# Kernel tuning notes

Hardware: AMD Instinct MI355X
Metric: run time of the kernel (lower is better)

The kernel has to match this reference:

```python
import jax, jax.numpy as jnp
import numpy as np

N_NODES = 40000
N_EDGES = 640000
F_IN = 128
HID = 128
N_CLASSES = 10
N_GRAPHS = 64


def _gcn_conv(x, row, col, norm, W, b, n_nodes):
    h = x @ W                                   # [N, H]
    msg = h[row] * norm[:, None]                # [E+N, H] gather + scale
    out = jax.ops.segment_sum(msg, col, num_segments=n_nodes)  # scatter-add
    return out + b


def setup_inputs() -> dict:
    key = jax.random.key(0)
    ks = jax.random.split(key, 8)
    x = jax.random.normal(ks[0], (N_NODES, F_IN), dtype=jnp.float32)
    edge_index = jax.random.randint(ks[1], (2, N_EDGES), 0, N_NODES, dtype=jnp.int32)
    batch = jnp.sort(jax.random.randint(ks[2], (N_NODES,), 0, N_GRAPHS, dtype=jnp.int32))
    s1 = 1.0 / np.sqrt(F_IN)
    s2 = 1.0 / np.sqrt(HID)
    W1 = jax.random.normal(ks[3], (F_IN, HID), dtype=jnp.float32) * s1
    W2 = jax.random.normal(ks[4], (HID, HID), dtype=jnp.float32) * s2
    W3 = jax.random.normal(ks[5], (HID, HID), dtype=jnp.float32) * s2
    Wl = jax.random.normal(ks[6], (HID, N_CLASSES), dtype=jnp.float32) * s2
    b1 = jnp.zeros((HID,), jnp.float32)
    b2 = jnp.zeros((HID,), jnp.float32)
    b3 = jnp.zeros((HID,), jnp.float32)
    bl = jnp.zeros((N_CLASSES,), jnp.float32)
    return {"x": x, "edge_index": edge_index, "batch": batch,
            "W1": W1, "b1": b1, "W2": W2, "b2": b2, "W3": W3, "b3": b3,
            "Wl": Wl, "bl": bl}


def reference(x, edge_index, batch, W1, b1, W2, b2, W3, b3, Wl, bl):
    n = x.shape[0]
    # add self-loops (PyG add_remaining_self_loops with weight 1)
    loops = jnp.arange(n, dtype=edge_index.dtype)
    row = jnp.concatenate([edge_index[0], loops])
    col = jnp.concatenate([edge_index[1], loops])
    w = jnp.ones(row.shape, dtype=x.dtype)
    # symmetric normalization: deg over target nodes incl. self-loops
    deg = jax.ops.segment_sum(w, col, num_segments=n)
    dis = jnp.where(deg > 0, jax.lax.rsqrt(deg), 0.0)
    norm = dis[row] * dis[col]                  # [E+N]

    h = jax.nn.relu(_gcn_conv(x, row, col, norm, W1, b1, n))
    h = jax.nn.relu(_gcn_conv(h, row, col, norm, W2, b2, n))
    h = jax.nn.relu(_gcn_conv(h, row, col, norm, W3, b3, n))

    # global mean pool over graph ids
    sums = jax.ops.segment_sum(h, batch, num_segments=N_GRAPHS)      # [G, H]
    cnts = jax.ops.segment_sum(jnp.ones((n,), h.dtype), batch, num_segments=N_GRAPHS)
    pooled = sums / jnp.maximum(cnts, 1.0)[:, None]
    # dropout(p=0.2) is identity in eval mode
    return pooled @ Wl + bl                     # [G, num_classes]
```

## Files before the change

kernel.cpp:

```cpp
#include <hip/hip_runtime.h>
#include <hip/hip_bf16.h>

#define N_NODES   40000
#define N_EDGES   640000
#define F         128
#define N_GRAPHS  64
#define N_CLASSES 10

typedef short bf16x8 __attribute__((ext_vector_type(8)));
typedef float f32x4  __attribute__((ext_vector_type(4)));

__device__ __forceinline__ unsigned short f2bf(float f) {
    union { float f; unsigned u; } v; v.f = f;
    unsigned r = v.u + 0x7fffu + ((v.u >> 16) & 1u);
    return (unsigned short)(r >> 16);
}
__device__ __forceinline__ float bflo(unsigned u) { return __uint_as_float(u << 16); }
__device__ __forceinline__ float bfhi(unsigned u) { return __uint_as_float(u & 0xffff0000u); }
__device__ __forceinline__ unsigned pack2(float a, float b) {
    return (unsigned)f2bf(a) | ((unsigned)f2bf(b) << 16);
}

#define APITCH 136

__global__ void wcvt_kernel(const float* __restrict__ W1, const float* __restrict__ W2,
                            const float* __restrict__ W3, unsigned short* __restrict__ Wt,
                            int* __restrict__ deg) {
    int idx = blockIdx.x * 256 + threadIdx.x;
    if (idx < N_NODES) deg[idx] = 0;
    int l = idx >> 14;
    int r = idx & 16383;
    int c = r >> 7, k = r & 127;
    const float* W = (l == 0) ? W1 : ((l == 1) ? W2 : W3);
    Wt[idx] = f2bf(W[k * 128 + c]);
}

__global__ __launch_bounds__(1024) void scan_kernel(
    const int* __restrict__ deg, int* __restrict__ rowptr,
    int* __restrict__ cursor, float* __restrict__ dis,
    float* __restrict__ pooled_zero) {
    __shared__ int wsum[16];
    __shared__ int tile_total_s;
    const int tid  = threadIdx.x;
    const int lane = tid & 63;
    const int wave = tid >> 6;

    for (int k = tid; k < N_GRAPHS * F + N_GRAPHS; k += 1024) pooled_zero[k] = 0.f;

    int running = 0;
    for (int t = 0; t < 10; ++t) {
        const int base = t * 4096 + tid * 4;
        int4 d = make_int4(0, 0, 0, 0);
        if (base < N_NODES) d = *(const int4*)(deg + base);
        const int sown = d.x + d.y + d.z + d.w;

        int s = sown;
#pragma unroll
        for (int off = 1; off < 64; off <<= 1) {
            int n = __shfl_up(s, off, 64);
            if (lane >= off) s += n;
        }
        if (lane == 63) wsum[wave] = s;
        __syncthreads();

        if (wave == 0) {
            int v = (lane < 16) ? wsum[lane] : 0;
#pragma unroll
            for (int off = 1; off < 16; off <<= 1) {
                int n = __shfl_up(v, off, 64);
                if (lane >= off) v += n;
            }
            if (lane < 16) wsum[lane] = v;
            if (lane == 15) tile_total_s = v;
        }
        __syncthreads();

        int excl = running + (wave ? wsum[wave - 1] : 0) + (s - sown);
        if (base < N_NODES) {
            int4 r;
            r.x = excl;
            r.y = r.x + d.x;
            r.z = r.y + d.y;
            r.w = r.z + d.z;
            *(int4*)(rowptr + base) = r;
            *(int4*)(cursor + base) = r;
            float4 di;
            di.x = rsqrtf((float)d.x + 1.0f);
            di.y = rsqrtf((float)d.y + 1.0f);
            di.z = rsqrtf((float)d.z + 1.0f);
            di.w = rsqrtf((float)d.w + 1.0f);
            *(float4*)(dis + base) = di;
        }
        running += tile_total_s;
        __syncthreads();
    }
}

__global__ void fill_kernel(const int* __restrict__ row, const int* __restrict__ col,
                            int* __restrict__ cursor, int* __restrict__ csr_src) {
    int e = blockIdx.x * 256 + threadIdx.x;
    if (e < N_EDGES) {
        int pos = atomicAdd(&cursor[col[e]], 1);
        csr_src[pos] = row[e];
    }
}

template<bool ABF16, bool RELU, bool SCALE, bool COUNT>
__global__ __launch_bounds__(256) void gemm_mfma(
    const void* __restrict__ Araw, const unsigned short* __restrict__ Wt,
    const float* __restrict__ bias, const float* __restrict__ dis,
    unsigned short* __restrict__ Hb,
    const int* __restrict__ cnt_col, int* __restrict__ cnt_deg) {
    __shared__ unsigned short As[64 * APITCH];
    __shared__ unsigned short Ws[128 * APITCH];
    const int tid  = threadIdx.x;
    const int row0 = blockIdx.x * 64;

    if (COUNT) {
        int t = (blockIdx.x * 256 + tid) * 4;
#pragma unroll
        for (int j = 0; j < 4; ++j) atomicAdd(&cnt_deg[cnt_col[t + j]], 1);
    }

    {
        const uint4* src = (const uint4*)Wt;
#pragma unroll
        for (int j = 0; j < 8; ++j) {
            int c4 = tid + j * 256;
            int c  = c4 >> 4;
            int o  = c4 & 15;
            *(uint4*)(Ws + c * APITCH + o * 8) = src[c4];
        }
    }
    if (ABF16) {
        const uint4* src = (const uint4*)Araw;
#pragma unroll
        for (int j = 0; j < 4; ++j) {
            int c4 = tid + j * 256;
            int r  = c4 >> 4;
            int p  = c4 & 15;
            int o  = p << 3;
            uint4 hv = src[(size_t)(row0 + r) * 16 + p];
            float f0 = bflo(hv.x), f1 = bfhi(hv.x), f2 = bflo(hv.y), f3 = bfhi(hv.y);
            float f4_ = bflo(hv.z), f5 = bfhi(hv.z), f6 = bflo(hv.w), f7 = bfhi(hv.w);
            if (bias) {
                float4 b0 = *(const float4*)(bias + o);
                float4 b1 = *(const float4*)(bias + o + 4);
                f0 += b0.x; f1 += b0.y; f2 += b0.z; f3 += b0.w;
                f4_ += b1.x; f5 += b1.y; f6 += b1.z; f7 += b1.w;
            }
            if (RELU) {
                f0 = fmaxf(f0, 0.f); f1 = fmaxf(f1, 0.f); f2 = fmaxf(f2, 0.f);
                f3 = fmaxf(f3, 0.f); f4_ = fmaxf(f4_, 0.f); f5 = fmaxf(f5, 0.f);
                f6 = fmaxf(f6, 0.f); f7 = fmaxf(f7, 0.f);
            }
            uint4 pk;
            pk.x = pack2(f0, f1); pk.y = pack2(f2, f3);
            pk.z = pack2(f4_, f5); pk.w = pack2(f6, f7);
            *(uint4*)(As + r * APITCH + o) = pk;
        }
    } else {
        const float* A = (const float*)Araw;
#pragma unroll
        for (int j = 0; j < 8; ++j) {
            int c4 = tid + j * 256;
            int r  = c4 >> 5;
            int o  = (c4 & 31) << 2;
            float4 v = *(const float4*)(A + (size_t)(row0 + r) * F + o);
            if (bias) {
                v.x += bias[o + 0]; v.y += bias[o + 1];
                v.z += bias[o + 2]; v.w += bias[o + 3];
            }
            if (RELU) {
                v.x = fmaxf(v.x, 0.f); v.y = fmaxf(v.y, 0.f);
                v.z = fmaxf(v.z, 0.f); v.w = fmaxf(v.w, 0.f);
            }
            uint2 p;
            p.x = pack2(v.x, v.y);
            p.y = pack2(v.z, v.w);
            *(uint2*)(As + r * APITCH + o) = p;
        }
    }
    __syncthreads();

    const int lane = tid & 63;
    const int wave = tid >> 6;
    const int m16  = lane & 15;
    const int quad = lane >> 4;

    f32x4 acc[8];
#pragma unroll
    for (int t = 0; t < 8; ++t) acc[t] = (f32x4)(0.0f);

#pragma unroll
    for (int ks = 0; ks < 128; ks += 32) {
        bf16x8 a = *(const bf16x8*)(As + (wave * 16 + m16) * APITCH + ks + quad * 8);
#pragma unroll
        for (int t = 0; t < 8; ++t) {
            bf16x8 b = *(const bf16x8*)(Ws + (t * 16 + m16) * APITCH + ks + quad * 8);
            acc[t] = __builtin_amdgcn_mfma_f32_16x16x32_bf16(a, b, acc[t], 0, 0, 0);
        }
    }

    const int rloc = wave * 16 + quad * 4;
    float sc[4];
#pragma unroll
    for (int rg = 0; rg < 4; ++rg) sc[rg] = SCALE ? dis[row0 + rloc + rg] : 1.0f;
#pragma unroll
    for (int t = 0; t < 8; ++t) {
        int col = t * 16 + m16;
#pragma unroll
        for (int rg = 0; rg < 4; ++rg)
            As[(rloc + rg) * APITCH + col] = f2bf(acc[t][rg] * sc[rg]);
    }
#pragma unroll
    for (int i = 0; i < 4; ++i) {
        int idx = lane + i * 64;
        int r   = idx >> 4;
        int p   = idx & 15;
        uint4 val = *(const uint4*)(As + (wave * 16 + r) * APITCH + p * 8);
        *((uint4*)(Hb + (size_t)(row0 + wave * 16 + r) * F) + p) = val;
    }
}

template <bool SCALED>
__global__ __launch_bounds__(256) void gather_kernel(
    const unsigned short* __restrict__ Hb, const int* __restrict__ csr_src,
    const int* __restrict__ rowptr, const int* __restrict__ deg,
    const float* __restrict__ dis, unsigned short* __restrict__ AGGb) {
    const int gid  = blockIdx.x * 256 + threadIdx.x;
    const int v    = gid >> 6;
    if (v >= N_NODES) return;
    const int lane = threadIdx.x & 63;
    const int part = lane & 15;
    const int quad = lane >> 4;

    const int start = rowptr[v];
    const int len   = deg[v];
    const uint4* Hp = (const uint4*)Hb + part;

    float acc[8];
#pragma unroll
    for (int i = 0; i < 8; ++i) acc[i] = 0.f;

    for (int j0 = 0; j0 < len; j0 += 64) {
        int m = len - j0; if (m > 64) m = 64;
        int nidx = (lane < m) ? csr_src[start + j0 + lane] : 0;
        for (int j = 0; j < m; j += 16) {
            int   r[4];
            float w[4];
            uint4 h[4];
#pragma unroll
            for (int u = 0; u < 4; ++u) {
                int  sl    = j + u * 4 + quad;
                bool valid = sl < m;
                r[u] = __shfl(nidx, valid ? sl : 0, 64);
                w[u] = valid ? (SCALED ? dis[r[u]] : 1.0f) : 0.0f;
            }
#pragma unroll
            for (int u = 0; u < 4; ++u) h[u] = Hp[(size_t)r[u] * 16];
#pragma unroll
            for (int u = 0; u < 4; ++u) {
                acc[0] = fmaf(bflo(h[u].x), w[u], acc[0]);
                acc[1] = fmaf(bfhi(h[u].x), w[u], acc[1]);
                acc[2] = fmaf(bflo(h[u].y), w[u], acc[2]);
                acc[3] = fmaf(bfhi(h[u].y), w[u], acc[3]);
                acc[4] = fmaf(bflo(h[u].z), w[u], acc[4]);
                acc[5] = fmaf(bfhi(h[u].z), w[u], acc[5]);
                acc[6] = fmaf(bflo(h[u].w), w[u], acc[6]);
                acc[7] = fmaf(bfhi(h[u].w), w[u], acc[7]);
            }
        }
    }

#pragma unroll
    for (int i = 0; i < 8; ++i) {
        acc[i] += __shfl_xor(acc[i], 16, 64);
        acc[i] += __shfl_xor(acc[i], 32, 64);
    }

    if (quad == 0) {
        float dc  = dis[v];
        float ws_ = SCALED ? dc : 1.0f;
        uint4 h = Hp[(size_t)v * 16];
        acc[0] = fmaf(bflo(h.x), ws_, acc[0]); acc[1] = fmaf(bfhi(h.x), ws_, acc[1]);
        acc[2] = fmaf(bflo(h.y), ws_, acc[2]); acc[3] = fmaf(bfhi(h.y), ws_, acc[3]);
        acc[4] = fmaf(bflo(h.z), ws_, acc[4]); acc[5] = fmaf(bfhi(h.z), ws_, acc[5]);
        acc[6] = fmaf(bflo(h.w), ws_, acc[6]); acc[7] = fmaf(bfhi(h.w), ws_, acc[7]);
        uint4 pk;
        pk.x = pack2(acc[0] * dc, acc[1] * dc);
        pk.y = pack2(acc[2] * dc, acc[3] * dc);
        pk.z = pack2(acc[4] * dc, acc[5] * dc);
        pk.w = pack2(acc[6] * dc, acc[7] * dc);
        *((uint4*)AGGb + (size_t)v * 16 + part) = pk;
    }
}

#define POOL_NODES 100
__global__ __launch_bounds__(256) void pool_kernel(
    const unsigned short* __restrict__ AGGb, const int* __restrict__ batch,
    const float* __restrict__ b3,
    float* __restrict__ pooled, float* __restrict__ cnt) {
    const int tid  = threadIdx.x;
    const int f4   = (tid & 31) << 2;
    const int slot = tid >> 5;
    const int base = blockIdx.x * POOL_NODES;
    const float4 bf = *(const float4*)(b3 + f4);

    float4 acc = make_float4(0.f, 0.f, 0.f, 0.f);
    float c = 0.f;
    int gcur = -1;
    for (int j = slot; j < POOL_NODES; j += 8) {
        int v = base + j;
        int g = batch[v];
        if (g != gcur) {
            if (gcur >= 0) {
                float* dst = pooled + gcur * F + f4;
                atomicAdd(dst + 0, acc.x); atomicAdd(dst + 1, acc.y);
                atomicAdd(dst + 2, acc.z); atomicAdd(dst + 3, acc.w);
                if (f4 == 0) atomicAdd(&cnt[gcur], c);
            }
            acc = make_float4(0.f, 0.f, 0.f, 0.f); c = 0.f; gcur = g;
        }
        uint2 a = *(const uint2*)(AGGb + (size_t)v * F + f4);
        acc.x += fmaxf(bflo(a.x) + bf.x, 0.f);
        acc.y += fmaxf(bfhi(a.x) + bf.y, 0.f);
        acc.z += fmaxf(bflo(a.y) + bf.z, 0.f);
        acc.w += fmaxf(bfhi(a.y) + bf.w, 0.f);
        c += 1.f;
    }
    if (gcur >= 0) {
        float* dst = pooled + gcur * F + f4;
        atomicAdd(dst + 0, acc.x); atomicAdd(dst + 1, acc.y);
        atomicAdd(dst + 2, acc.z); atomicAdd(dst + 3, acc.w);
        if (f4 == 0) atomicAdd(&cnt[gcur], c);
    }
}

__global__ void head_kernel(const float* __restrict__ pooled,
                            const float* __restrict__ cnt,
                            const float* __restrict__ Wl,
                            const float* __restrict__ bl,
                            float* __restrict__ out) {
    int tid = threadIdx.x;
    if (tid >= N_GRAPHS * N_CLASSES) return;
    int g = tid / N_CLASSES, c = tid % N_CLASSES;
    float acc = 0.f;
    for (int ff = 0; ff < F; ++ff)
        acc += pooled[g * F + ff] * Wl[ff * N_CLASSES + c];
    out[g * N_CLASSES + c] = acc / fmaxf(cnt[g], 1.f) + bl[c];
}

extern "C" void kernel_launch(void* const* d_in, const int* in_sizes, int n_in,
                              void* d_out, int out_size, void* d_ws, size_t ws_size,
                              hipStream_t stream) {
    const float* x    = (const float*)d_in[0];
    const int*   ei   = (const int*)d_in[1];
    const int*   bat  = (const int*)d_in[2];
    const float* W1   = (const float*)d_in[3];
    const float* b1   = (const float*)d_in[4];
    const float* W2   = (const float*)d_in[5];
    const float* b2   = (const float*)d_in[6];
    const float* W3   = (const float*)d_in[7];
    const float* b3   = (const float*)d_in[8];
    const float* Wl   = (const float*)d_in[9];
    const float* bl   = (const float*)d_in[10];
    float* out = (float*)d_out;

    const int* row = ei;
    const int* col = ei + N_EDGES;

    float*          ws      = (float*)d_ws;
    float*          dis     = ws;
    unsigned short* Hb      = (unsigned short*)(dis + N_NODES);
    unsigned short* AGGb    = Hb + (size_t)N_NODES * F;
    float*          pooled  = (float*)(AGGb + (size_t)N_NODES * F);
    float*          cnt     = pooled + N_GRAPHS * F;
    int*            deg     = (int*)(cnt + N_GRAPHS);
    int*            rowptr  = deg + N_NODES;
    int*            cursor  = rowptr + N_NODES;
    int*            csr_src = cursor + N_NODES;
    unsigned short* Wtb     = (unsigned short*)(csr_src + N_EDGES);

    const int edgeGrid   = (N_EDGES + 255) / 256;
    const int gemmGrid   = N_NODES / 64;
    const int gatherGrid = (N_NODES * 64) / 256;

    wcvt_kernel<<<192, 256, 0, stream>>>(W1, W2, W3, Wtb, deg);

    gemm_mfma<false, false, false, true><<<gemmGrid, 256, 0, stream>>>(
        x, Wtb, nullptr, nullptr, Hb, col, deg);
    scan_kernel<<<1, 1024, 0, stream>>>(deg, rowptr, cursor, dis, pooled);
    fill_kernel<<<edgeGrid, 256, 0, stream>>>(row, col, cursor, csr_src);
    gather_kernel<true><<<gatherGrid, 256, 0, stream>>>(Hb, csr_src, rowptr, deg, dis, AGGb);

    gemm_mfma<true, true, true, false><<<gemmGrid, 256, 0, stream>>>(
        AGGb, Wtb + 16384, b1, dis, Hb, nullptr, nullptr);
    gather_kernel<false><<<gatherGrid, 256, 0, stream>>>(Hb, csr_src, rowptr, deg, dis, AGGb);

    gemm_mfma<true, true, true, false><<<gemmGrid, 256, 0, stream>>>(
        AGGb, Wtb + 32768, b2, dis, Hb, nullptr, nullptr);
    gather_kernel<false><<<gatherGrid, 256, 0, stream>>>(Hb, csr_src, rowptr, deg, dis, AGGb);

    pool_kernel<<<N_NODES / POOL_NODES, 256, 0, stream>>>(AGGb, bat, b3, pooled, cnt);
    head_kernel<<<1, N_GRAPHS * N_CLASSES, 0, stream>>>(pooled, cnt, Wl, bl, out);
}
```

Baseline: 301.5 us.

## Parallelize degree scan across blocks and fuse classifier head into pool

The single-block 1024-thread prefix scan becomes a 40-block scan. Each block publishes its chunk sum, then spins on a global ticket until all blocks arrive before computing its base offset. The head kernel is folded into pool_kernel through a last-block-done ticket, which removes one launch. The grid-wide spin barrier assumes all 40 blocks are co-resident, and the tickets must be reset each run by wcvt_kernel.

```diff
diff --git a/kernel.cpp b/kernel.cpp
--- a/kernel.cpp
+++ b/kernel.cpp
@@ -25,9 +25,10 @@
 
 __global__ void wcvt_kernel(const float* __restrict__ W1, const float* __restrict__ W2,
                             const float* __restrict__ W3, unsigned short* __restrict__ Wt,
-                            int* __restrict__ deg) {
+                            int* __restrict__ deg, int* __restrict__ tks) {
     int idx = blockIdx.x * 256 + threadIdx.x;
     if (idx < N_NODES) deg[idx] = 0;
+    if (idx < 2) tks[idx] = 0;
     int l = idx >> 14;
     int r = idx & 16383;
     int c = r >> 7, k = r & 127;
@@ -35,64 +36,66 @@
     Wt[idx] = f2bf(W[k * 128 + c]);
 }
 
-__global__ __launch_bounds__(1024) void scan_kernel(
+#define SCAN_BLOCKS 40
+#define SCAN_CHUNK  1000
+__global__ __launch_bounds__(256) void scan_kernel(
     const int* __restrict__ deg, int* __restrict__ rowptr,
     int* __restrict__ cursor, float* __restrict__ dis,
-    float* __restrict__ pooled_zero) {
-    __shared__ int wsum[16];
-    __shared__ int tile_total_s;
+    float* __restrict__ pooled_zero, int* __restrict__ chunkSum,
+    int* __restrict__ ticket) {
+    __shared__ int wpart[4];
+    __shared__ int blockBase;
     const int tid  = threadIdx.x;
     const int lane = tid & 63;
     const int wave = tid >> 6;
-
-    for (int k = tid; k < N_GRAPHS * F + N_GRAPHS; k += 1024) pooled_zero[k] = 0.f;
-
-    int running = 0;
-    for (int t = 0; t < 10; ++t) {
-        const int base = t * 4096 + tid * 4;
-        int4 d = make_int4(0, 0, 0, 0);
-        if (base < N_NODES) d = *(const int4*)(deg + base);
-        const int sown = d.x + d.y + d.z + d.w;
-
-        int s = sown;
-#pragma unroll
-        for (int off = 1; off < 64; off <<= 1) {
-            int n = __shfl_up(s, off, 64);
-            if (lane >= off) s += n;
-        }
-        if (lane == 63) wsum[wave] = s;
-        __syncthreads();
-
-        if (wave == 0) {
-            int v = (lane < 16) ? wsum[lane] : 0;
-#pragma unroll
-            for (int off = 1; off < 16; off <<= 1) {
-                int n = __shfl_up(v, off, 64);
-                if (lane >= off) v += n;
-            }
-            if (lane < 16) wsum[lane] = v;
-            if (lane == 15) tile_total_s = v;
-        }
-        __syncthreads();
-
-        int excl = running + (wave ? wsum[wave - 1] : 0) + (s - sown);
-        if (base < N_NODES) {
-            int4 r;
-            r.x = excl;
-            r.y = r.x + d.x;
-            r.z = r.y + d.y;
-            r.w = r.z + d.z;
-            *(int4*)(rowptr + base) = r;
-            *(int4*)(cursor + base) = r;
-            float4 di;
-            di.x = rsqrtf((float)d.x + 1.0f);
-            di.y = rsqrtf((float)d.y + 1.0f);
-            di.z = rsqrtf((float)d.z + 1.0f);
-            di.w = rsqrtf((float)d.w + 1.0f);
-            *(float4*)(dis + base) = di;
-        }
-        running += tile_total_s;
-        __syncthreads();
+    const int b    = blockIdx.x;
+    const int base = b * SCAN_CHUNK;
+
+    for (int k = b * 256 + tid; k < N_GRAPHS * F + N_GRAPHS; k += SCAN_BLOCKS * 256)
+        pooled_zero[k] = 0.f;
+
+    int4 d = make_int4(0, 0, 0, 0);
+    if (tid < 250) d = *(const int4*)(deg + base + tid * 4);
+    const int sown = d.x + d.y + d.z + d.w;
+
+    int s = sown;
+#pragma unroll
+    for (int off = 1; off < 64; off <<= 1) {
+        int n = __shfl_up(s, off, 64);
+        if (lane >= off) s += n;
+    }
+    if (lane == 63) wpart[wave] = s;
+    __syncthreads();
+
+    if (tid == 0) {
+        int run = 0;
+#pragma unroll
+        for (int w = 0; w < 4; ++w) { int t = wpart[w]; wpart[w] = run; run += t; }
+        atomicExch(&chunkSum[b], run);
+        __threadfence();
+        atomicAdd(ticket, 1);
+        while (atomicAdd(ticket, 0) < SCAN_BLOCKS) { }
+        int bp = 0;
+        for (int i = 0; i < b; ++i) bp += atomicAdd(&chunkSum[i], 0);
+        blockBase = bp;
+    }
+    __syncthreads();
+
+    if (tid < 250) {
+        int excl = blockBase + wpart[wave] + (s - sown);
+        int4 r;
+        r.x = excl;
+        r.y = r.x + d.x;
+        r.z = r.y + d.y;
+        r.w = r.z + d.z;
+        *(int4*)(rowptr + base + tid * 4) = r;
+        *(int4*)(cursor + base + tid * 4) = r;
+        float4 di;
+        di.x = rsqrtf((float)d.x + 1.0f);
+        di.y = rsqrtf((float)d.y + 1.0f);
+        di.z = rsqrtf((float)d.z + 1.0f);
+        di.w = rsqrtf((float)d.w + 1.0f);
+        *(float4*)(dis + base + tid * 4) = di;
     }
 }
 
@@ -299,8 +302,13 @@
 #define POOL_NODES 100
 __global__ __launch_bounds__(256) void pool_kernel(
     const unsigned short* __restrict__ AGGb, const int* __restrict__ batch,
-    const float* __restrict__ b3,
-    float* __restrict__ pooled, float* __restrict__ cnt) {
+    const float* __restrict__ b3, float* __restrict__ pooled,
+    float* __restrict__ cnt, const float* __restrict__ Wl,
+    const float* __restrict__ bl, float* __restrict__ out,
+    int* __restrict__ ticket2) {
+    __shared__ float plds[N_GRAPHS * F];
+    __shared__ float clds[N_GRAPHS];
+    __shared__ int lastflag;
     const int tid  = threadIdx.x;
     const int f4   = (tid & 31) << 2;
     const int slot = tid >> 5;
@@ -335,20 +343,28 @@
         atomicAdd(dst + 2, acc.z); atomicAdd(dst + 3, acc.w);
         if (f4 == 0) atomicAdd(&cnt[gcur], c);
     }
-}
-
-__global__ void head_kernel(const float* __restrict__ pooled,
-                            const float* __restrict__ cnt,
-                            const float* __restrict__ Wl,
-                            const float* __restrict__ bl,
-                            float* __restrict__ out) {
-    int tid = threadIdx.x;
-    if (tid >= N_GRAPHS * N_CLASSES) return;
-    int g = tid / N_CLASSES, c = tid % N_CLASSES;
-    float acc = 0.f;
-    for (int ff = 0; ff < F; ++ff)
-        acc += pooled[g * F + ff] * Wl[ff * N_CLASSES + c];
-    out[g * N_CLASSES + c] = acc / fmaxf(cnt[g], 1.f) + bl[c];
+
+    __threadfence();
+    __syncthreads();
+    if (tid == 0) {
+        int old = atomicAdd(ticket2, 1);
+        lastflag = (old == (int)gridDim.x - 1);
+    }
+    __syncthreads();
+    if (!lastflag) return;
+
+    for (int k = tid; k < N_GRAPHS * F; k += 256)
+        plds[k] = atomicAdd(&pooled[k], 0.f);
+    if (tid < N_GRAPHS) clds[tid] = atomicAdd(&cnt[tid], 0.f);
+    __syncthreads();
+
+    for (int oidx = tid; oidx < N_GRAPHS * N_CLASSES; oidx += 256) {
+        int g = oidx / N_CLASSES, cc = oidx % N_CLASSES;
+        float a = 0.f;
+        for (int f = 0; f < F; ++f)
+            a += plds[g * F + f] * Wl[f * N_CLASSES + cc];
+        out[oidx] = a / fmaxf(clds[g], 1.f) + bl[cc];
+    }
 }
 
 extern "C" void kernel_launch(void* const* d_in, const int* in_sizes, int n_in,
@@ -381,16 +397,19 @@
     int*            cursor  = rowptr + N_NODES;
     int*            csr_src = cursor + N_NODES;
     unsigned short* Wtb     = (unsigned short*)(csr_src + N_EDGES);
+    int*            chunkSum= (int*)(Wtb + 3 * 16384);
+    int*            tks     = chunkSum + SCAN_BLOCKS;
 
     const int edgeGrid   = (N_EDGES + 255) / 256;
     const int gemmGrid   = N_NODES / 64;
     const int gatherGrid = (N_NODES * 64) / 256;
 
-    wcvt_kernel<<<192, 256, 0, stream>>>(W1, W2, W3, Wtb, deg);
+    wcvt_kernel<<<192, 256, 0, stream>>>(W1, W2, W3, Wtb, deg, tks);
 
     gemm_mfma<false, false, false, true><<<gemmGrid, 256, 0, stream>>>(
         x, Wtb, nullptr, nullptr, Hb, col, deg);
-    scan_kernel<<<1, 1024, 0, stream>>>(deg, rowptr, cursor, dis, pooled);
+    scan_kernel<<<SCAN_BLOCKS, 256, 0, stream>>>(deg, rowptr, cursor, dis,
+                                                 pooled, chunkSum, &tks[0]);
     fill_kernel<<<edgeGrid, 256, 0, stream>>>(row, col, cursor, csr_src);
     gather_kernel<true><<<gatherGrid, 256, 0, stream>>>(Hb, csr_src, rowptr, deg, dis, AGGb);
 
@@ -402,6 +421,6 @@
         AGGb, Wtb + 32768, b2, dis, Hb, nullptr, nullptr);
     gather_kernel<false><<<gatherGrid, 256, 0, stream>>>(Hb, csr_src, rowptr, deg, dis, AGGb);
 
-    pool_kernel<<<N_NODES / POOL_NODES, 256, 0, stream>>>(AGGb, bat, b3, pooled, cnt);
-    head_kernel<<<1, N_GRAPHS * N_CLASSES, 0, stream>>>(pooled, cnt, Wl, bl, out);
-}
+    pool_kernel<<<N_NODES / POOL_NODES, 256, 0, stream>>>(
+        AGGb, bat, b3, pooled, cnt, Wl, bl, out, &tks[1]);
+}
```

Result: slower. 308.5 us (+2.3%).
